# Kernel tuning notes

Hardware: AMD Instinct MI355X
Metric: run time of the kernel (lower is better)

The kernel has to match this reference:

```python
import jax, jax.numpy as jnp
import numpy as np

BN_EPS = 1e-3  # keras BatchNormalization default epsilon


def batch_norm(x):
    # Fresh keras BatchNorm in training mode: gamma=1, beta=0, batch stats over axis 0
    mean = jnp.mean(x, axis=0, keepdims=True)
    var = jnp.var(x, axis=0, keepdims=True)
    return (x - mean) * jax.lax.rsqrt(var + BN_EPS)


def setup_inputs() -> dict:
    key = jax.random.key(0)
    k1, k2, k3 = jax.random.split(key, 3)
    N, D = 100000, 512
    x1 = jax.random.normal(k1, (N, D), dtype=jnp.float32)
    x2 = jax.random.normal(k2, (N, D), dtype=jnp.float32)
    # glorot_uniform for [D, D] kernel
    limit = np.sqrt(6.0 / (D + D)).astype(np.float32)
    kernel = jax.random.uniform(k3, (D, D), dtype=jnp.float32, minval=-limit, maxval=limit)
    return {"x1": x1, "x2": x2, "kernel": kernel}


def reference(x1, x2, kernel):
    b1 = batch_norm(x1)  # [N, D]
    b2 = batch_norm(x2)  # [N, D]
    gate = jax.nn.relu(jnp.tanh(b1 @ kernel))  # [N, D]; dropout_rate=0 -> no dropout
    out = jnp.tanh(b2 * (1.0 - gate) + b1 * gate)
    return out
```

## Files before the change

### kernel.cpp

```cpp
#include <hip/hip_runtime.h>
#include <hip/hip_bf16.h>
#include <hip/hip_fp16.h>
#include <stdint.h>

#define N_ROWS 100000
#define DCOLS 512
#define BN_EPS 1e-3f
#define PB 256

typedef __attribute__((ext_vector_type(8))) _Float16 f16x8;
typedef __attribute__((ext_vector_type(4))) float f32x4;
typedef __attribute__((ext_vector_type(4))) unsigned short u16x4;
typedef __attribute__((ext_vector_type(4))) unsigned int u32x4;

__device__ inline float fast_tanh(float x) {
  float e = __expf(2.0f * x);
  return (e - 1.0f) / (e + 1.0f);
}
__device__ inline void gld16(const void* g, void* l) {
  __builtin_amdgcn_global_load_lds(
      (const __attribute__((address_space(1))) void*)g,
      (__attribute__((address_space(3))) void*)l, 16, 0, 0);
}
__device__ inline unsigned int h2u(__half2 h) {
  unsigned int u;
  __builtin_memcpy(&u, &h, 4);
  return u;
}

__device__ inline void split8h(const float4& v0, const float4& v1,
                               u32x4& hi, u32x4& lo) {
  __half2 h0 = __floats2half2_rn(v0.x, v0.y);
  __half2 h1 = __floats2half2_rn(v0.z, v0.w);
  __half2 h2 = __floats2half2_rn(v1.x, v1.y);
  __half2 h3 = __floats2half2_rn(v1.z, v1.w);
  __half2 l0 = __floats2half2_rn(v0.x - __low2float(h0), v0.y - __high2float(h0));
  __half2 l1 = __floats2half2_rn(v0.z - __low2float(h1), v0.w - __high2float(h1));
  __half2 l2 = __floats2half2_rn(v1.x - __low2float(h2), v1.y - __high2float(h2));
  __half2 l3 = __floats2half2_rn(v1.z - __low2float(h3), v1.w - __high2float(h3));
  hi = (u32x4){h2u(h0), h2u(h1), h2u(h2), h2u(h3)};
  lo = (u32x4){h2u(l0), h2u(l1), h2u(l2), h2u(l3)};
}

__global__ __launch_bounds__(256) void k_stats_partial(
    const float* __restrict__ x1, const float* __restrict__ x2,
    float* __restrict__ psum, float* __restrict__ psq) {
  const int CH = (N_ROWS + PB - 1) / PB;
  int bx = blockIdx.x;
  int arr = blockIdx.y;
  const float* x = arr ? x2 : x1;
  int r0 = bx * CH;
  int r1 = min(N_ROWS, r0 + CH);
  int c0 = threadIdx.x * 2;
  float s0 = 0.f, s1 = 0.f, q0 = 0.f, q1 = 0.f;
#pragma unroll 8
  for (int r = r0; r < r1; ++r) {
    float2 v = *(const float2*)(x + (size_t)r * DCOLS + c0);
    s0 += v.x; s1 += v.y;
    q0 += v.x * v.x; q1 += v.y * v.y;
  }
  size_t base = ((size_t)(arr * PB + bx)) * DCOLS + c0;
  psum[base] = s0; psum[base + 1] = s1;
  psq[base]  = q0; psq[base + 1]  = q1;
}

__global__ __launch_bounds__(512) void k_stats_final(
    const float* __restrict__ psum, const float* __restrict__ psq,
    float* __restrict__ stats) {
  int a = blockIdx.x;
  int c = threadIdx.x;
  float sa[8], qa[8];
#pragma unroll
  for (int u = 0; u < 8; ++u) { sa[u] = 0.f; qa[u] = 0.f; }
  for (int b = 0; b < PB; b += 8) {
#pragma unroll
    for (int u = 0; u < 8; ++u) {
      size_t base = ((size_t)(a * PB + b + u)) * DCOLS + c;
      sa[u] += psum[base];
      qa[u] += psq[base];
    }
  }
  float s = ((sa[0]+sa[1])+(sa[2]+sa[3]))+((sa[4]+sa[5])+(sa[6]+sa[7]));
  float q = ((qa[0]+qa[1])+(qa[2]+qa[3]))+((qa[4]+qa[5])+(qa[6]+qa[7]));
  float inv = 1.0f / (float)N_ROWS;
  float mean = s * inv;
  float var = q * inv - mean * mean;
  float scale = rsqrtf(var + BN_EPS);
  stats[a * 1024 + c] = scale;
  stats[a * 1024 + 512 + c] = -mean * scale;
}

__global__ __launch_bounds__(256) void k_prepw(
    const float* __restrict__ wk, const float* __restrict__ stats,
    u32x4* __restrict__ wf) {
  int gid = blockIdx.x * 256 + threadIdx.x;
  int j = gid & 511;
  int kg = gid >> 9;
  int k0 = kg * 8;
  unsigned short h[8];
#pragma unroll
  for (int u = 0; u < 8; ++u) {
    float w = wk[(size_t)(k0 + u) * DCOLS + j] * stats[k0 + u];
    __half hh = __float2half_rn(w);
    h[u] = __half_as_ushort(hh);
  }
  int slice = k0 >> 5;
  int lr = (k0 >> 3) & 3;
  int lane = (lr << 4) | (j & 15);
  int g = j >> 4;
  int idx = slice * 2048 + g * 64 + lane;
  u16x4* ph = (u16x4*)&wf[idx];
  u16x4 h0 = {h[0], h[1], h[2], h[3]};
  u16x4 h1 = {h[4], h[5], h[6], h[7]};
  ph[0] = h0; ph[1] = h1;
}

__global__ __launch_bounds__(512) void k_c_partial(
    const float* __restrict__ wk, const float* __restrict__ stats,
    float* __restrict__ cpart) {
  int b = blockIdx.x;
  int j = threadIdx.x;
  const float* negms1 = stats + 512;
  float acc = 0.f;
#pragma unroll
  for (int u = 0; u < 8; ++u) {
    int k = b * 8 + u;
    acc += negms1[k] * wk[(size_t)k * DCOLS + j];
  }
  cpart[b * DCOLS + j] = acc;
}

__global__ __launch_bounds__(512) void k_c_final(
    const float* __restrict__ cpart, float* __restrict__ cvec) {
  int j = threadIdx.x;
  float a = 0.f;
  for (int b = 0; b < 64; ++b) a += cpart[b * DCOLS + j];
  cvec[j] = a;
}

__global__ __launch_bounds__(512, 4) void k_main(
    const float* __restrict__ x1, const float* __restrict__ x2,
    const float* __restrict__ stats, const float* __restrict__ cvec,
    const u32x4* __restrict__ wf, float* __restrict__ out) {
  __shared__ char smem[65536];

  const int tid = threadIdx.x;
  const int lane = tid & 63;
  const int wv = tid >> 6;
  const int wr = wv >> 2;
  const int wc = wv & 3;

  const int xcd = blockIdx.x & 7;
  const int wgid = xcd * 391 + (blockIdx.x >> 3);
  const int panel = wgid >> 2;
  const int q = wgid & 3;
  const int row0 = panel * 128;
  const int col0 = q * 128;

  const float* scale1 = stats;
  const float* negms1 = stats + 512;
  const float* scale2 = stats + 1024;
  const float* negms2 = stats + 1536;

  const int ra = lane & 15;
  const int rq = lane >> 4;

  const float* aptr[2];
  int aoff[2];
#pragma unroll
  for (int u = 0; u < 2; ++u) {
    int f = (tid >> 6) + 8 * u;
    int kk = f >> 3, fm = f & 7;
    int row = row0 + fm * 16 + (tid & 15);
    row = min(row, N_ROWS - 1);
    aptr[u] = x1 + (size_t)row * DCOLS + kk * 32 + ((tid >> 4) & 3) * 8;
    aoff[u] = f * 1024 + (tid & 63) * 16;
  }
  float4 av0[2], av1[2];
  auto loadA = [&](int s) {
#pragma unroll
    for (int u = 0; u < 2; ++u) {
      const float* p = aptr[u] + s * 64;
      av0[u] = *(const float4*)p;
      av1[u] = *(const float4*)(p + 4);
    }
  };
  auto writeA = [&]() {
#pragma unroll
    for (int u = 0; u < 2; ++u) {
      u32x4 hi, lo;
      split8h(av0[u], av1[u], hi, lo);
      *(u32x4*)(smem + aoff[u]) = hi;
      *(u32x4*)(smem + 16384 + aoff[u]) = lo;
    }
  };

  auto stageB = [&](int s, int b) {
#pragma unroll
    for (int e = 0; e < 2; ++e) {
      int id = wv * 2 + e;
      int kk = id >> 3;
      int g = id & 7;
      const u32x4* src =
          wf + (size_t)(s * 2 + kk) * 2048 + (size_t)(q * 8 + g) * 64 + lane;
      gld16(src, smem + 32768 + b * 16384 + id * 1024);
    }
  };

  f32x4 acc[4][2];
#pragma unroll
  for (int fn = 0; fn < 2; ++fn) {
    float cj = cvec[col0 + wc * 32 + fn * 16 + ra];
#pragma unroll
    for (int fm = 0; fm < 4; ++fm) acc[fm][fn] = (f32x4){cj, cj, cj, cj};
  }

  loadA(0);
  stageB(0, 0);
  writeA();
  asm volatile("s_waitcnt vmcnt(0) lgkmcnt(0)" ::: "memory");
  __builtin_amdgcn_s_barrier();
  __builtin_amdgcn_sched_barrier(0);

  for (int s = 0; s < 8; ++s) {
    const int buf = s & 1;
    if (s < 7) {
      loadA(s + 1);
      stageB(s + 1, buf ^ 1);
    }
    __builtin_amdgcn_sched_barrier(0);

#pragma unroll
    for (int kk = 0; kk < 2; ++kk) {
      f16x8 ah[4], al[4], bf[2];
#pragma unroll
      for (int fm = 0; fm < 4; ++fm) {
        int off = (kk * 8 + wr * 4 + fm) * 1024 + lane * 16;
        ah[fm] = *(const f16x8*)(smem + off);
        al[fm] = *(const f16x8*)(smem + 16384 + off);
      }
#pragma unroll
      for (int fn = 0; fn < 2; ++fn) {
        int pb = kk * 8 + wc * 2 + fn;
        bf[fn] = *(const f16x8*)(smem + 32768 + buf * 16384 + pb * 1024 +
                                 lane * 16);
      }
      __builtin_amdgcn_s_setprio(1);
#pragma unroll
      for (int fm = 0; fm < 4; ++fm)
#pragma unroll
        for (int fn = 0; fn < 2; ++fn)
          acc[fm][fn] = __builtin_amdgcn_mfma_f32_16x16x32_f16(
              ah[fm], bf[fn], acc[fm][fn], 0, 0, 0);
#pragma unroll
      for (int fm = 0; fm < 4; ++fm)
#pragma unroll
        for (int fn = 0; fn < 2; ++fn)
          acc[fm][fn] = __builtin_amdgcn_mfma_f32_16x16x32_f16(
              al[fm], bf[fn], acc[fm][fn], 0, 0, 0);
      __builtin_amdgcn_s_setprio(0);
    }

    asm volatile("s_waitcnt lgkmcnt(0)" ::: "memory");
    __builtin_amdgcn_s_barrier();
    __builtin_amdgcn_sched_barrier(0);

    if (s < 7) {
      writeA();
      asm volatile("s_waitcnt vmcnt(0) lgkmcnt(0)" ::: "memory");
      __builtin_amdgcn_s_barrier();
      __builtin_amdgcn_sched_barrier(0);
    }
  }

  float s1j[2], n1j[2], s2j[2], n2j[2];
#pragma unroll
  for (int fn = 0; fn < 2; ++fn) {
    int j = col0 + wc * 32 + fn * 16 + ra;
    s1j[fn] = scale1[j]; n1j[fn] = negms1[j];
    s2j[fn] = scale2[j]; n2j[fn] = negms2[j];
  }
#pragma unroll
  for (int fm = 0; fm < 4; ++fm) {
#pragma unroll
    for (int r = 0; r < 4; ++r) {
      int n = row0 + wr * 64 + fm * 16 + rq * 4 + r;
      if (n < N_ROWS) {
#pragma unroll
        for (int fn = 0; fn < 2; ++fn) {
          int j = col0 + wc * 32 + fn * 16 + ra;
          float c = acc[fm][fn][r];
          float tt = fast_tanh(c);
          float g = fmaxf(tt, 0.0f);
          size_t idx = (size_t)n * DCOLS + j;
          float b1v = fmaf(x1[idx], s1j[fn], n1j[fn]);
          float b2v = fmaf(x2[idx], s2j[fn], n2j[fn]);
          out[idx] = fast_tanh(b2v + g * (b1v - b2v));
        }
      }
    }
  }
}

extern "C" void kernel_launch(void* const* d_in, const int* in_sizes, int n_in,
                              void* d_out, int out_size, void* d_ws, size_t ws_size,
                              hipStream_t stream) {
  const float* x1 = (const float*)d_in[0];
  const float* x2 = (const float*)d_in[1];
  const float* wk = (const float*)d_in[2];
  float* out = (float*)d_out;
  char* ws = (char*)d_ws;

  if (ws_size < (size_t)(4u << 20)) return;

  float* psum  = (float*)ws;
  float* psq   = (float*)(ws + (1 << 20));
  float* stats = (float*)(ws + (2 << 20));
  float* cpart = (float*)(ws + (2 << 20) + (16 << 10));
  float* cvec  = (float*)(ws + (2 << 20) + (160 << 10));
  u32x4* wf    = (u32x4*)(ws + (3 << 20));

  k_stats_partial<<<dim3(PB, 2), 256, 0, stream>>>(x1, x2, psum, psq);
  k_stats_final<<<2, 512, 0, stream>>>(psum, psq, stats);
  k_prepw<<<128, 256, 0, stream>>>(wk, stats, wf);
  k_c_partial<<<64, 512, 0, stream>>>(wk, stats, cpart);
  k_c_final<<<1, 512, 0, stream>>>(cpart, cvec);

  const int nblocks = 8 * 391;
  k_main<<<nblocks, 512, 0, stream>>>(x1, x2, stats, cvec, wf, out);
}
```

Measured before the change: 334.2 us.

## Keep A fragments in registers, split per-wave rows, drop A LDS staging

Each wave now owns 16 rows across the full 128-column tile and loads its x1 fragment straight from global memory into registers. The fp16 hi/lo split now happens in registers, so the A tile no longer goes through LDS, and the extra barrier and writeA pass per k-step are gone. LDS shrinks to 32 KB holding only double-buffered B, and the main loop is fully unrolled with a vmcnt-based wait. fast_tanh switches to a reciprocal-based form. The cost is that each wave reads all 8 B fragments from LDS per k-substep, a wave's A data is no longer shared with other waves, and more registers are live.

```diff
diff --git a/kernel.cpp b/kernel.cpp
--- a/kernel.cpp
+++ b/kernel.cpp
@@ -1,5 +1,4 @@
 #include <hip/hip_runtime.h>
-#include <hip/hip_bf16.h>
 #include <hip/hip_fp16.h>
 #include <stdint.h>
 
@@ -15,7 +14,7 @@
 
 __device__ inline float fast_tanh(float x) {
   float e = __expf(2.0f * x);
-  return (e - 1.0f) / (e + 1.0f);
+  return 1.0f - 2.0f * __builtin_amdgcn_rcpf(e + 1.0f);
 }
 __device__ inline void gld16(const void* g, void* l) {
   __builtin_amdgcn_global_load_lds(
@@ -27,9 +26,14 @@
   __builtin_memcpy(&u, &h, 4);
   return u;
 }
+__device__ inline f16x8 u2f(const u32x4& u) {
+  f16x8 h;
+  __builtin_memcpy(&h, &u, 16);
+  return h;
+}
 
 __device__ inline void split8h(const float4& v0, const float4& v1,
-                               u32x4& hi, u32x4& lo) {
+                               f16x8& hi8, f16x8& lo8) {
   __half2 h0 = __floats2half2_rn(v0.x, v0.y);
   __half2 h1 = __floats2half2_rn(v0.z, v0.w);
   __half2 h2 = __floats2half2_rn(v1.x, v1.y);
@@ -38,8 +42,10 @@
   __half2 l1 = __floats2half2_rn(v0.z - __low2float(h1), v0.w - __high2float(h1));
   __half2 l2 = __floats2half2_rn(v1.x - __low2float(h2), v1.y - __high2float(h2));
   __half2 l3 = __floats2half2_rn(v1.z - __low2float(h3), v1.w - __high2float(h3));
-  hi = (u32x4){h2u(h0), h2u(h1), h2u(h2), h2u(h3)};
-  lo = (u32x4){h2u(l0), h2u(l1), h2u(l2), h2u(l3)};
+  u32x4 hi = (u32x4){h2u(h0), h2u(h1), h2u(h2), h2u(h3)};
+  u32x4 lo = (u32x4){h2u(l0), h2u(l1), h2u(l2), h2u(l3)};
+  hi8 = u2f(hi);
+  lo8 = u2f(lo);
 }
 
 __global__ __launch_bounds__(256) void k_stats_partial(
@@ -142,13 +148,13 @@
     const float* __restrict__ x1, const float* __restrict__ x2,
     const float* __restrict__ stats, const float* __restrict__ cvec,
     const u32x4* __restrict__ wf, float* __restrict__ out) {
-  __shared__ char smem[65536];
+  __shared__ char smem[32768];
 
   const int tid = threadIdx.x;
   const int lane = tid & 63;
   const int wv = tid >> 6;
-  const int wr = wv >> 2;
-  const int wc = wv & 3;
+  const int ra = lane & 15;
+  const int rq = lane >> 4;
 
   const int xcd = blockIdx.x & 7;
   const int wgid = xcd * 391 + (blockIdx.x >> 3);
@@ -157,146 +163,111 @@
   const int row0 = panel * 128;
   const int col0 = q * 128;
 
+  int arow = row0 + wv * 16 + ra;
+  arow = min(arow, N_ROWS - 1);
+  const float* abase = x1 + (size_t)arow * DCOLS + rq * 8;
+
+  const u32x4* bsrc[2];
+  int bdst[2];
+#pragma unroll
+  for (int e = 0; e < 2; ++e) {
+    int id = wv * 2 + e;
+    int kk = id >> 3, g = id & 7;
+    bsrc[e] = wf + (size_t)kk * 2048 + (size_t)(q * 8 + g) * 64 + lane;
+    bdst[e] = id * 1024;
+  }
+
+  f32x4 acc[8];
+#pragma unroll
+  for (int g = 0; g < 8; ++g) {
+    float cj = cvec[col0 + g * 16 + ra];
+    acc[g] = (f32x4){cj, cj, cj, cj};
+  }
+
+  float4 av[2][4];
+
+  auto stageB = [&](int s, int buf) {
+#pragma unroll
+    for (int e = 0; e < 2; ++e)
+      gld16(bsrc[e] + (size_t)s * 2 * 2048, smem + buf * 16384 + bdst[e]);
+  };
+  auto loadA = [&](int s, int pset) {
+    const float* p = abase + s * 64;
+    av[pset][0] = *(const float4*)(p);
+    av[pset][1] = *(const float4*)(p + 4);
+    av[pset][2] = *(const float4*)(p + 32);
+    av[pset][3] = *(const float4*)(p + 36);
+  };
+
+  stageB(0, 0);
+  asm volatile("" ::: "memory");
+  loadA(0, 0);
+  asm volatile("s_waitcnt vmcnt(4)" ::: "memory");
+  __builtin_amdgcn_s_barrier();
+  __builtin_amdgcn_sched_barrier(0);
+
+#pragma unroll
+  for (int s = 0; s < 8; ++s) {
+    const int p = s & 1;
+    if (s < 7) {
+      stageB(s + 1, p ^ 1);
+      asm volatile("" ::: "memory");
+      loadA(s + 1, p ^ 1);
+      __builtin_amdgcn_sched_barrier(0);
+    }
+#pragma unroll
+    for (int kk = 0; kk < 2; ++kk) {
+      f16x8 bf[8];
+#pragma unroll
+      for (int g = 0; g < 8; ++g)
+        bf[g] = *(const f16x8*)(smem + p * 16384 + (kk * 8 + g) * 1024 +
+                                lane * 16);
+      f16x8 ah, al;
+      split8h(av[p][kk * 2], av[p][kk * 2 + 1], ah, al);
+      __builtin_amdgcn_s_setprio(1);
+#pragma unroll
+      for (int g = 0; g < 8; ++g)
+        acc[g] = __builtin_amdgcn_mfma_f32_16x16x32_f16(ah, bf[g], acc[g],
+                                                        0, 0, 0);
+#pragma unroll
+      for (int g = 0; g < 8; ++g)
+        acc[g] = __builtin_amdgcn_mfma_f32_16x16x32_f16(al, bf[g], acc[g],
+                                                        0, 0, 0);
+      __builtin_amdgcn_s_setprio(0);
+    }
+    if (s < 7) {
+      asm volatile("s_waitcnt vmcnt(4)" ::: "memory");
+      __builtin_amdgcn_s_barrier();
+      __builtin_amdgcn_sched_barrier(0);
+    }
+  }
+
   const float* scale1 = stats;
   const float* negms1 = stats + 512;
   const float* scale2 = stats + 1024;
   const float* negms2 = stats + 1536;
 
-  const int ra = lane & 15;
-  const int rq = lane >> 4;
-
-  const float* aptr[2];
-  int aoff[2];
-#pragma unroll
-  for (int u = 0; u < 2; ++u) {
-    int f = (tid >> 6) + 8 * u;
-    int kk = f >> 3, fm = f & 7;
-    int row = row0 + fm * 16 + (tid & 15);
-    row = min(row, N_ROWS - 1);
-    aptr[u] = x1 + (size_t)row * DCOLS + kk * 32 + ((tid >> 4) & 3) * 8;
-    aoff[u] = f * 1024 + (tid & 63) * 16;
-  }
-  float4 av0[2], av1[2];
-  auto loadA = [&](int s) {
-#pragma unroll
-    for (int u = 0; u < 2; ++u) {
-      const float* p = aptr[u] + s * 64;
-      av0[u] = *(const float4*)p;
-      av1[u] = *(const float4*)(p + 4);
-    }
-  };
-  auto writeA = [&]() {
-#pragma unroll
-    for (int u = 0; u < 2; ++u) {
-      u32x4 hi, lo;
-      split8h(av0[u], av1[u], hi, lo);
-      *(u32x4*)(smem + aoff[u]) = hi;
-      *(u32x4*)(smem + 16384 + aoff[u]) = lo;
-    }
-  };
-
-  auto stageB = [&](int s, int b) {
-#pragma unroll
-    for (int e = 0; e < 2; ++e) {
-      int id = wv * 2 + e;
-      int kk = id >> 3;
-      int g = id & 7;
-      const u32x4* src =
-          wf + (size_t)(s * 2 + kk) * 2048 + (size_t)(q * 8 + g) * 64 + lane;
-      gld16(src, smem + 32768 + b * 16384 + id * 1024);
-    }
-  };
-
-  f32x4 acc[4][2];
-#pragma unroll
-  for (int fn = 0; fn < 2; ++fn) {
-    float cj = cvec[col0 + wc * 32 + fn * 16 + ra];
-#pragma unroll
-    for (int fm = 0; fm < 4; ++fm) acc[fm][fn] = (f32x4){cj, cj, cj, cj};
-  }
-
-  loadA(0);
-  stageB(0, 0);
-  writeA();
-  asm volatile("s_waitcnt vmcnt(0) lgkmcnt(0)" ::: "memory");
-  __builtin_amdgcn_s_barrier();
-  __builtin_amdgcn_sched_barrier(0);
-
-  for (int s = 0; s < 8; ++s) {
-    const int buf = s & 1;
-    if (s < 7) {
-      loadA(s + 1);
-      stageB(s + 1, buf ^ 1);
-    }
-    __builtin_amdgcn_sched_barrier(0);
-
-#pragma unroll
-    for (int kk = 0; kk < 2; ++kk) {
-      f16x8 ah[4], al[4], bf[2];
-#pragma unroll
-      for (int fm = 0; fm < 4; ++fm) {
-        int off = (kk * 8 + wr * 4 + fm) * 1024 + lane * 16;
-        ah[fm] = *(const f16x8*)(smem + off);
-        al[fm] = *(const f16x8*)(smem + 16384 + off);
-      }
-#pragma unroll
-      for (int fn = 0; fn < 2; ++fn) {
-        int pb = kk * 8 + wc * 2 + fn;
-        bf[fn] = *(const f16x8*)(smem + 32768 + buf * 16384 + pb * 1024 +
-                                 lane * 16);
-      }
-      __builtin_amdgcn_s_setprio(1);
-#pragma unroll
-      for (int fm = 0; fm < 4; ++fm)
-#pragma unroll
-        for (int fn = 0; fn < 2; ++fn)
-          acc[fm][fn] = __builtin_amdgcn_mfma_f32_16x16x32_f16(
-              ah[fm], bf[fn], acc[fm][fn], 0, 0, 0);
-#pragma unroll
-      for (int fm = 0; fm < 4; ++fm)
-#pragma unroll
-        for (int fn = 0; fn < 2; ++fn)
-          acc[fm][fn] = __builtin_amdgcn_mfma_f32_16x16x32_f16(
-              al[fm], bf[fn], acc[fm][fn], 0, 0, 0);
-      __builtin_amdgcn_s_setprio(0);
-    }
-
-    asm volatile("s_waitcnt lgkmcnt(0)" ::: "memory");
-    __builtin_amdgcn_s_barrier();
-    __builtin_amdgcn_sched_barrier(0);
-
-    if (s < 7) {
-      writeA();
-      asm volatile("s_waitcnt vmcnt(0) lgkmcnt(0)" ::: "memory");
-      __builtin_amdgcn_s_barrier();
-      __builtin_amdgcn_sched_barrier(0);
-    }
-  }
-
-  float s1j[2], n1j[2], s2j[2], n2j[2];
-#pragma unroll
-  for (int fn = 0; fn < 2; ++fn) {
-    int j = col0 + wc * 32 + fn * 16 + ra;
-    s1j[fn] = scale1[j]; n1j[fn] = negms1[j];
-    s2j[fn] = scale2[j]; n2j[fn] = negms2[j];
-  }
-#pragma unroll
-  for (int fm = 0; fm < 4; ++fm) {
-#pragma unroll
-    for (int r = 0; r < 4; ++r) {
-      int n = row0 + wr * 64 + fm * 16 + rq * 4 + r;
-      if (n < N_ROWS) {
-#pragma unroll
-        for (int fn = 0; fn < 2; ++fn) {
-          int j = col0 + wc * 32 + fn * 16 + ra;
-          float c = acc[fm][fn][r];
-          float tt = fast_tanh(c);
-          float g = fmaxf(tt, 0.0f);
-          size_t idx = (size_t)n * DCOLS + j;
-          float b1v = fmaf(x1[idx], s1j[fn], n1j[fn]);
-          float b2v = fmaf(x2[idx], s2j[fn], n2j[fn]);
-          out[idx] = fast_tanh(b2v + g * (b1v - b2v));
-        }
+  float s1j[8], n1j[8], s2j[8], n2j[8];
+#pragma unroll
+  for (int g = 0; g < 8; ++g) {
+    int j = col0 + g * 16 + ra;
+    s1j[g] = scale1[j]; n1j[g] = negms1[j];
+    s2j[g] = scale2[j]; n2j[g] = negms2[j];
+  }
+#pragma unroll
+  for (int r = 0; r < 4; ++r) {
+    int n = row0 + wv * 16 + rq * 4 + r;
+    if (n < N_ROWS) {
+#pragma unroll
+      for (int g = 0; g < 8; ++g) {
+        int j = col0 + g * 16 + ra;
+        float c = acc[g][r];
+        float tt = fast_tanh(c);
+        float gt = fmaxf(tt, 0.0f);
+        size_t idx = (size_t)n * DCOLS + j;
+        float b1v = fmaf(x1[idx], s1j[g], n1j[g]);
+        float b2v = fmaf(x2[idx], s2j[g], n2j[g]);
+        out[idx] = fast_tanh(b2v + gt * (b1v - b2v));
       }
     }
   }
```

Result: faster. 304.6 us (-8.9%).
